# Performance work log

Measured on AMD Instinct MI355X. Metric: run time of the kernel, lower is better.

## Reference

```python
import jax, jax.numpy as jnp
import numpy as np
from jax import lax

STRIDE = (1, 1)
PADDING = ((1, 1), (1, 1))
DILATION = (1, 1)


def setup_inputs() -> dict:
    key = jax.random.key(0)
    k1, k2 = jax.random.split(key)
    input = jax.random.normal(k1, (32, 128, 56, 56), dtype=jnp.float32)
    weight = jax.random.normal(k2, (256, 128, 3, 3), dtype=jnp.float32)
    bias = jnp.zeros((256,), dtype=jnp.float32)
    return {"input": input, "weight": weight, "bias": bias}


def reference(input, weight, bias):
    # The original builds the conv's dense matrix via conv2d on an identity
    # basis and then matmuls; that is mathematically identical to a direct
    # conv2d (the map is linear), plus the broadcast bias.
    out = lax.conv_general_dilated(
        input, weight,
        window_strides=STRIDE,
        padding=PADDING,
        rhs_dilation=DILATION,
        dimension_numbers=("NCHW", "OIHW", "NCHW"),
    )
    return out + bias[None, :, None, None]
```

## Files before the change

### kernel.cpp

```cpp
#include <hip/hip_runtime.h>
#include <hip/hip_bf16.h>
#include <stdint.h>


typedef __attribute__((ext_vector_type(8))) short bf16x8;
typedef __attribute__((ext_vector_type(8))) unsigned short ushort8;
typedef __attribute__((ext_vector_type(4))) float f32x4;

#define HW       56
#define SPATIAL  3136
#define C_IN     128
#define K_OUT    256
#define GEMM_K   1152
#define GEMM_N   100352

#define PHW      58
#define PIMG     3364
#define PADTOT_AL 107656

#define BM       256
#define BN       128
#define NTILE    18
#define BUFH     24576

__device__ __forceinline__ unsigned short f2bf(float f) {
    union { float f; unsigned int u; } v; v.f = f;
    unsigned int u = v.u + 0x7FFFu + ((v.u >> 16) & 1u);
    return (unsigned short)(u >> 16);
}

__device__ __forceinline__ void gload16(const unsigned short* g, unsigned short* l) {
    __builtin_amdgcn_global_load_lds(
        (const __attribute__((address_space(1))) unsigned int*)(g),
        (__attribute__((address_space(3))) unsigned int*)(l),
        16, 0, 0);
}

__global__ void wtrans_kernel(const float* __restrict__ w, unsigned short* __restrict__ w3) {
    int idx = blockIdx.x * 256 + threadIdx.x;
    int rc   = idx / 18432;
    int rem  = idx % 18432;
    int tap  = rem / 2048;
    int rem2 = rem % 2048;
    int cc   = rem2 / 512;
    int s    = rem2 % 512;
    int l    = s >> 3, j = s & 7;
    int ko   = rc * 16 + (l & 15);
    int c    = cc * 32 + ((l >> 4) << 3) + j;
    w3[idx] = f2bf(w[(ko * C_IN + c) * 9 + tap]);
}

__global__ __launch_bounds__(256)
void border_zero(unsigned short* __restrict__ pad) {
    int idx = blockIdx.x * 256 + threadIdx.x;
    if (idx >= 29184) return;
    int cc  = idx / 7296;
    int r   = idx % 7296;
    int img = r / 228;
    int p   = r % 228;
    int pos;
    if (p < 58)       pos = p;
    else if (p < 116) pos = 57 * PHW + (p - 58);
    else { int i = p - 116; pos = (1 + (i >> 1)) * PHW + (i & 1) * 57; }
    unsigned short* d = pad + (size_t)cc * PADTOT_AL * 32
                      + ((size_t)img * PIMG + pos) * 32;
    const ushort8 z = (ushort8){0,0,0,0,0,0,0,0};
    *reinterpret_cast<ushort8*>(d)      = z;
    *reinterpret_cast<ushort8*>(d + 8)  = z;
    *reinterpret_cast<ushort8*>(d + 16) = z;
    *reinterpret_cast<ushort8*>(d + 24) = z;
}

__global__ __launch_bounds__(256)
void intrans_kernel(const float* __restrict__ in, unsigned short* __restrict__ pad) {
    __shared__ __attribute__((aligned(16))) unsigned short l[56 * 136];
    const int bx = blockIdx.x;
    const int n = bx / HW, h = bx % HW;
    const int tid = threadIdx.x;
    const float* src = in + (size_t)n * C_IN * SPATIAL + h * HW;
    #pragma unroll
    for (int i = 0; i < 28; ++i) {
        int idx = i * 256 + tid;
        int c = idx / HW, w = idx % HW;
        l[w * 136 + c] = f2bf(src[(size_t)c * SPATIAL + w]);
    }
    __syncthreads();
    const int prow = n * PIMG + (h + 1) * PHW;
    #pragma unroll
    for (int j = 0; j < 4; ++j) {
        int chunk = j * 256 + tid;
        if (chunk < 896) {
            int w = chunk >> 4, c8 = chunk & 15;
            int cc = c8 >> 2, sub = c8 & 3;
            unsigned short* dst = pad + (size_t)cc * PADTOT_AL * 32
                                + (size_t)(prow + w + 1) * 32 + sub * 8;
            *reinterpret_cast<ushort8*>(dst) =
                *reinterpret_cast<const ushort8*>(&l[w * 136 + c8 * 8]);
        }
    }
}

__global__ __launch_bounds__(512, 1)
void conv_m201(const unsigned short* __restrict__ pad,
               const unsigned short* __restrict__ w3,
               const float* __restrict__ bias,
               float* __restrict__ out) {
    __shared__ __attribute__((aligned(16))) unsigned short lds[3 * BUFH];

    const int tid  = threadIdx.x;
    const int wave = tid >> 6;
    const int lane = tid & 63;
    const int la   = lane & 15;
    const int lkh  = lane >> 4;

    const int bid = blockIdx.x;
    const int nt  = (bid & 7) * 98 + (bid >> 3);
    const int g0  = nt * BN;

    const int wr = wave >> 1, wc = wave & 1;

    const unsigned short* aw0 = w3 + (size_t)(wave * 2 + 0) * 18432 + lane * 8;
    const unsigned short* aw1 = w3 + (size_t)(wave * 2 + 1) * 18432 + lane * 8;
    const unsigned short* bsrc;
    {
        int col = g0 + wave * 16 + la;
        int img = col / SPATIAL;
        int pos = col - img * SPATIAL;
        int oh  = pos / HW, ow = pos - oh * HW;
        bsrc = pad + (size_t)(img * PIMG + (oh + 1) * PHW + (ow + 1)) * 32 + lkh * 8;
    }

    f32x4 acc[4][4];
    #pragma unroll
    for (int i = 0; i < 4; ++i)
        #pragma unroll
        for (int j = 0; j < 4; ++j)
            acc[i][j] = (f32x4){0.f, 0.f, 0.f, 0.f};

    auto STAGE = [&](int tn, int kc) {
        const int tap = tn >> 1;
        const int cc  = (tn & 1) * 2 + kc;
        const int dr = tap / 3 - 1, dsx = tap % 3 - 1;
        unsigned short* dst = &lds[(tn % 3) * BUFH];
        gload16(aw0 + (size_t)(tap * 4 + cc) * 512, dst + (wave * 4 + kc) * 512);
        gload16(aw1 + (size_t)(tap * 4 + cc) * 512, dst + (wave * 4 + 2 + kc) * 512);
        gload16(bsrc + (size_t)cc * PADTOT_AL * 32 + (dr * PHW + dsx) * 32,
                dst + 16384 + (wave * 2 + kc) * 512);
    };

    STAGE(0, 0); STAGE(0, 1);
    STAGE(1, 0); STAGE(1, 1);
    asm volatile("s_waitcnt vmcnt(6)" ::: "memory");
    __builtin_amdgcn_s_barrier();

    #pragma unroll
    for (int t = 0; t < NTILE; ++t) {
        const unsigned short* Ab = &lds[(t % 3) * BUFH];
        #pragma unroll
        for (int ks = 0; ks < 2; ++ks) {
            bf16x8 af[4], bv[4];
            #pragma unroll
            for (int mi = 0; mi < 4; ++mi)
                af[mi] = *reinterpret_cast<const bf16x8*>(
                    &Ab[((wr * 4 + mi) * 2 + ks) * 512 + lane * 8]);
            #pragma unroll
            for (int nj = 0; nj < 4; ++nj)
                bv[nj] = *reinterpret_cast<const bf16x8*>(
                    &Ab[16384 + ((wc * 4 + nj) * 2 + ks) * 512 + lane * 8]);

            if (t + 2 < NTILE) STAGE(t + 2, ks);

            __builtin_amdgcn_s_barrier();
            asm volatile("s_waitcnt lgkmcnt(0)" ::: "memory");
            __builtin_amdgcn_sched_barrier(0);

            __builtin_amdgcn_s_setprio(1);
            #pragma unroll
            for (int mi = 0; mi < 4; ++mi)
                #pragma unroll
                for (int nj = 0; nj < 4; ++nj)
                    acc[mi][nj] = __builtin_amdgcn_mfma_f32_16x16x32_bf16(
                        af[mi], bv[nj], acc[mi][nj], 0, 0, 0);
            __builtin_amdgcn_s_setprio(0);

            if (ks == 1 && t + 1 < NTILE)
                asm volatile("s_waitcnt vmcnt(6)" ::: "memory");
            __builtin_amdgcn_s_barrier();
        }
    }

    #pragma unroll
    for (int mi = 0; mi < 4; ++mi) {
        const int mb = wr * 64 + mi * 16 + lkh * 4;
        const f32x4 bv4 = *reinterpret_cast<const f32x4*>(&bias[mb]);
        #pragma unroll
        for (int nj = 0; nj < 4; ++nj) {
            const int gcol = g0 + wc * 64 + nj * 16;
            const int n2 = gcol / SPATIAL;
            const int p2 = gcol - n2 * SPATIAL + la;
            float* op = out + ((size_t)(n2 * K_OUT + mb)) * SPATIAL + p2;
            op[0]                   = acc[mi][nj][0] + bv4[0];
            op[SPATIAL]             = acc[mi][nj][1] + bv4[1];
            op[2 * SPATIAL]         = acc[mi][nj][2] + bv4[2];
            op[3 * (size_t)SPATIAL] = acc[mi][nj][3] + bv4[3];
        }
    }
}

#define LDK 40
__global__ __launch_bounds__(256)
void conv_mfma_fallback(const float* __restrict__ in,
                        const float* __restrict__ wraw,
                        const float* __restrict__ bias,
                        float* __restrict__ out) {
    __shared__ __attribute__((aligned(16))) unsigned short lA[128 * LDK];
    __shared__ __attribute__((aligned(16))) unsigned short lB[128 * LDK];
    const int tid = threadIdx.x;
    const int m0  = blockIdx.y * 128;
    const int g0  = blockIdx.x * 128;
    const int wave = tid >> 6, lane = tid & 63;
    const int wr = wave >> 1, wc = wave & 1;
    const int la = lane & 15, lkh = lane >> 4, lk = lkh * 8;

    f32x4 acc[4][4];
    #pragma unroll
    for (int i = 0; i < 4; ++i)
        #pragma unroll
        for (int j = 0; j < 4; ++j)
            acc[i][j] = (f32x4){0.f, 0.f, 0.f, 0.f};

    const int jj = tid & 127;
    const int kb = (tid >> 7) * 16;
    const int g = g0 + jj;
    const int nimg = g / SPATIAL;
    const int pos  = g % SPATIAL;
    const int oh = pos / HW, ow = pos % HW;

    for (int tap = 0; tap < 9; ++tap) {
        const int dr = tap / 3 - 1, dsx = tap % 3 - 1;
        const int ih = oh + dr, iw = ow + dsx;
        const bool valid = ((unsigned)ih < HW) && ((unsigned)iw < HW);
        const float* src = in + ((nimg * C_IN) * HW + ih) * HW + iw;
        for (int c0 = 0; c0 < C_IN; c0 += 32) {
            #pragma unroll
            for (int i = 0; i < 2; ++i) {
                const int ch = tid * 2 + i;
                const int row = ch >> 2;
                const int kp = (ch & 3) * 8;
                ushort8 v;
                #pragma unroll
                for (int e = 0; e < 8; ++e)
                    v[e] = f2bf(wraw[((m0 + row) * C_IN + c0 + kp + e) * 9 + tap]);
                *reinterpret_cast<ushort8*>(&lA[row * LDK + kp]) = v;
            }
            {
                ushort8 v0, v1;
                #pragma unroll
                for (int i = 0; i < 8; ++i)
                    v0[i] = f2bf(valid ? src[(c0 + kb + i) * SPATIAL] : 0.f);
                #pragma unroll
                for (int i = 0; i < 8; ++i)
                    v1[i] = f2bf(valid ? src[(c0 + kb + 8 + i) * SPATIAL] : 0.f);
                *reinterpret_cast<ushort8*>(&lB[jj * LDK + kb])     = v0;
                *reinterpret_cast<ushort8*>(&lB[jj * LDK + kb + 8]) = v1;
            }
            __syncthreads();
            bf16x8 af[4], bv[4];
            #pragma unroll
            for (int f = 0; f < 4; ++f) {
                af[f] = *reinterpret_cast<const bf16x8*>(&lA[(wr * 64 + f * 16 + la) * LDK + lk]);
                bv[f] = *reinterpret_cast<const bf16x8*>(&lB[(wc * 64 + f * 16 + la) * LDK + lk]);
            }
            #pragma unroll
            for (int fi = 0; fi < 4; ++fi)
                #pragma unroll
                for (int fj = 0; fj < 4; ++fj)
                    acc[fi][fj] = __builtin_amdgcn_mfma_f32_16x16x32_bf16(
                        af[fi], bv[fj], acc[fi][fj], 0, 0, 0);
            __syncthreads();
        }
    }
    const int mbase = m0 + wr * 64;
    const int cbase = g0 + wc * 64;
    #pragma unroll
    for (int fi = 0; fi < 4; ++fi) {
        float bvv[4];
        #pragma unroll
        for (int r = 0; r < 4; ++r)
            bvv[r] = bias[mbase + fi * 16 + lkh * 4 + r];
        #pragma unroll
        for (int fj = 0; fj < 4; ++fj) {
            const int gcol = cbase + fj * 16 + la;
            const int n2 = gcol / SPATIAL;
            const int p2 = gcol % SPATIAL;
            float* op = out + (size_t)(n2 * K_OUT) * SPATIAL + p2;
            #pragma unroll
            for (int r = 0; r < 4; ++r)
                op[(size_t)(mbase + fi * 16 + lkh * 4 + r) * SPATIAL] = acc[fi][fj][r] + bvv[r];
        }
    }
}

extern "C" void kernel_launch(void* const* d_in, const int* in_sizes, int n_in,
                              void* d_out, int out_size, void* d_ws, size_t ws_size,
                              hipStream_t stream) {
    const float* in   = (const float*)d_in[0];
    const float* w    = (const float*)d_in[1];
    const float* bias = (const float*)d_in[2];
    float* out = (float*)d_out;

    const size_t pad_halves = 4ull * PADTOT_AL * 32ull;
    const size_t need_bytes = (pad_halves + 294912ull) * 2ull;

    if (ws_size >= need_bytes) {
        unsigned short* pad = (unsigned short*)d_ws;
        unsigned short* w3  = pad + pad_halves;
        border_zero<<<114, 256, 0, stream>>>(pad);
        wtrans_kernel<<<294912 / 256, 256, 0, stream>>>(w, w3);
        intrans_kernel<<<32 * HW, 256, 0, stream>>>(in, pad);
        conv_m201<<<GEMM_N / BN, 512, 0, stream>>>(pad, w3, bias, out);
    } else {
        dim3 grid(GEMM_N / 128, K_OUT / 128);
        conv_mfma_fallback<<<grid, 256, 0, stream>>>(in, w, bias, out);
    }
}
```

Baseline: 105.6 us.

## Double-buffer LDS fragment reads in registers to overlap with MFMA

After: 100.4 us. 1.05x faster.

```diff
diff --git a/kernel.cpp b/kernel.cpp
--- a/kernel.cpp
+++ b/kernel.cpp
@@ -101,7 +101,7 @@
 }
 
 __global__ __launch_bounds__(512, 1)
-void conv_m201(const unsigned short* __restrict__ pad,
+void conv_pipe(const unsigned short* __restrict__ pad,
                const unsigned short* __restrict__ w3,
                const float* __restrict__ bias,
                float* __restrict__ out) {
@@ -148,45 +148,73 @@
                 dst + 16384 + (wave * 2 + kc) * 512);
     };
 
+    bf16x8 a0[4], b0[4], a1[4], b1[4];
+
+    auto READ0 = [&](int tn, int ks) {
+        const unsigned short* Ab = &lds[(tn % 3) * BUFH];
+        #pragma unroll
+        for (int mi = 0; mi < 4; ++mi)
+            a0[mi] = *reinterpret_cast<const bf16x8*>(
+                &Ab[((wr * 4 + mi) * 2 + ks) * 512 + lane * 8]);
+        #pragma unroll
+        for (int nj = 0; nj < 4; ++nj)
+            b0[nj] = *reinterpret_cast<const bf16x8*>(
+                &Ab[16384 + ((wc * 4 + nj) * 2 + ks) * 512 + lane * 8]);
+    };
+    auto READ1 = [&](int tn, int ks) {
+        const unsigned short* Ab = &lds[(tn % 3) * BUFH];
+        #pragma unroll
+        for (int mi = 0; mi < 4; ++mi)
+            a1[mi] = *reinterpret_cast<const bf16x8*>(
+                &Ab[((wr * 4 + mi) * 2 + ks) * 512 + lane * 8]);
+        #pragma unroll
+        for (int nj = 0; nj < 4; ++nj)
+            b1[nj] = *reinterpret_cast<const bf16x8*>(
+                &Ab[16384 + ((wc * 4 + nj) * 2 + ks) * 512 + lane * 8]);
+    };
+
     STAGE(0, 0); STAGE(0, 1);
     STAGE(1, 0); STAGE(1, 1);
     asm volatile("s_waitcnt vmcnt(6)" ::: "memory");
     __builtin_amdgcn_s_barrier();
+    asm volatile("" ::: "memory");
+    READ0(0, 0);
 
     #pragma unroll
     for (int t = 0; t < NTILE; ++t) {
-        const unsigned short* Ab = &lds[(t % 3) * BUFH];
-        #pragma unroll
-        for (int ks = 0; ks < 2; ++ks) {
-            bf16x8 af[4], bv[4];
-            #pragma unroll
-            for (int mi = 0; mi < 4; ++mi)
-                af[mi] = *reinterpret_cast<const bf16x8*>(
-                    &Ab[((wr * 4 + mi) * 2 + ks) * 512 + lane * 8]);
+        READ1(t, 1);
+        if (t + 2 < NTILE) STAGE(t + 2, 0);
+        asm volatile("s_waitcnt lgkmcnt(8)" ::: "memory");
+        __builtin_amdgcn_sched_barrier(0);
+        __builtin_amdgcn_s_setprio(1);
+        #pragma unroll
+        for (int mi = 0; mi < 4; ++mi)
             #pragma unroll
             for (int nj = 0; nj < 4; ++nj)
-                bv[nj] = *reinterpret_cast<const bf16x8*>(
-                    &Ab[16384 + ((wc * 4 + nj) * 2 + ks) * 512 + lane * 8]);
-
-            if (t + 2 < NTILE) STAGE(t + 2, ks);
-
+                acc[mi][nj] = __builtin_amdgcn_mfma_f32_16x16x32_bf16(
+                    a0[mi], b0[nj], acc[mi][nj], 0, 0, 0);
+        __builtin_amdgcn_s_setprio(0);
+
+        if (t + 2 < NTILE) STAGE(t + 2, 1);
+        asm volatile("s_waitcnt lgkmcnt(0)" ::: "memory");
+        __builtin_amdgcn_sched_barrier(0);
+        if (t + 1 < NTILE) {
+            if (t + 2 < NTILE)
+                asm volatile("s_waitcnt vmcnt(6)" ::: "memory");
+            else
+                asm volatile("s_waitcnt vmcnt(0)" ::: "memory");
             __builtin_amdgcn_s_barrier();
-            asm volatile("s_waitcnt lgkmcnt(0)" ::: "memory");
-            __builtin_amdgcn_sched_barrier(0);
-
-            __builtin_amdgcn_s_setprio(1);
-            #pragma unroll
-            for (int mi = 0; mi < 4; ++mi)
-                #pragma unroll
-                for (int nj = 0; nj < 4; ++nj)
-                    acc[mi][nj] = __builtin_amdgcn_mfma_f32_16x16x32_bf16(
-                        af[mi], bv[nj], acc[mi][nj], 0, 0, 0);
-            __builtin_amdgcn_s_setprio(0);
-
-            if (ks == 1 && t + 1 < NTILE)
-                asm volatile("s_waitcnt vmcnt(6)" ::: "memory");
-            __builtin_amdgcn_s_barrier();
-        }
+            asm volatile("" ::: "memory");
+            READ0(t + 1, 0);
+        }
+        __builtin_amdgcn_s_setprio(1);
+        #pragma unroll
+        for (int mi = 0; mi < 4; ++mi)
+            #pragma unroll
+            for (int nj = 0; nj < 4; ++nj)
+                acc[mi][nj] = __builtin_amdgcn_mfma_f32_16x16x32_bf16(
+                    a1[mi], b1[nj], acc[mi][nj], 0, 0, 0);
+        __builtin_amdgcn_s_setprio(0);
     }
 
     #pragma unroll
@@ -318,7 +346,7 @@
         border_zero<<<114, 256, 0, stream>>>(pad);
         wtrans_kernel<<<294912 / 256, 256, 0, stream>>>(w, w3);
         intrans_kernel<<<32 * HW, 256, 0, stream>>>(in, pad);
-        conv_m201<<<GEMM_N / BN, 512, 0, stream>>>(pad, w3, bias, out);
+        conv_pipe<<<GEMM_N / BN, 512, 0, stream>>>(pad, w3, bias, out);
     } else {
         dim3 grid(GEMM_N / 128, K_OUT / 128);
         conv_mfma_fallback<<<grid, 256, 0, stream>>>(in, w, bias, out);
```
